# Kernel tuning notes

Measured on AMD Instinct MI355X. Metric: run time of the kernel, lower is better.

The kernel has to match this reference:

```python
import jax, jax.numpy as jnp
import numpy as np

B, T, Q, H = 128, 50, 1024, 256
MAX_STEP = 50
TEMP = 0.5
SUP_W, DIST_W, EMBED_W, LOSS_WEIGHT = 1.0, 0.01, 1.0, 1.0
BLUR, DIAMETER, REACH, SCALING, P = 0.005, 1.0, 500.0, 0.5, 2
NEG = -1e9


def _softmin(eps, C, h):
    # h: log-weights + potential/eps over the second axis of C
    return -eps * jax.nn.logsumexp(h[None, :] - C / eps, axis=1)


def _sqcost(u, v):
    sq = jnp.sum(u * u, -1)[:, None] + jnp.sum(v * v, -1)[None, :] - 2.0 * (u @ v.T)
    return 0.5 * jnp.maximum(sq, 0.0)  # geomloss p=2 cost: |x-y|^2 / 2


def sinkhorn_divergence(x, y):
    # geomloss SamplesLoss('sinkhorn', p=2, blur=0.005, diameter=1, reach=500),
    # tensorized, debiased, unbalanced, eps-scaling schedule.
    N, M = x.shape[0], y.shape[0]
    a_log = jnp.full((N,), -np.log(float(N)), dtype=x.dtype)
    b_log = jnp.full((M,), -np.log(float(M)), dtype=x.dtype)
    Cxy, Cyx = _sqcost(x, y), _sqcost(y, x)
    Cxx, Cyy = _sqcost(x, x), _sqcost(y, y)
    rho = REACH ** P
    eps_final = BLUR ** P
    eps_list = []
    e = DIAMETER ** P
    while e > eps_final:
        eps_list.append(e)
        e = e * (SCALING ** P)
    eps_list.append(eps_final)
    f_ab = jnp.zeros((N,), x.dtype)
    g_ab = jnp.zeros((M,), x.dtype)
    f_aa = jnp.zeros((N,), x.dtype)
    g_bb = jnp.zeros((M,), x.dtype)
    for eps in eps_list:  # static schedule (~9 steps)
        damp = 1.0 / (1.0 + eps / rho)
        ft = damp * _softmin(eps, Cxy, b_log + g_ab / eps)
        gt = damp * _softmin(eps, Cyx, a_log + f_ab / eps)
        faa = 0.5 * (f_aa + damp * _softmin(eps, Cxx, a_log + f_aa / eps))
        gbb = 0.5 * (g_bb + damp * _softmin(eps, Cyy, b_log + g_bb / eps))
        f_ab, g_ab, f_aa, g_bb = ft, gt, faa, gbb
    w = rho + eps_final / 2.0  # UnbalancedWeight
    a_w, b_w = jnp.exp(a_log), jnp.exp(b_log)
    return (jnp.sum(a_w * w * (jnp.exp(-f_aa / rho) - jnp.exp(-f_ab / rho)))
            + jnp.sum(b_w * w * (jnp.exp(-g_bb / rho) - jnp.exp(-g_ab / rho))))


def _forward(lc, lt, le, ltc, ltt, lte, ohs, oht, ods, odt, batch):
    p_c, p_t, p_e = lc / TEMP, lt / TEMP, le / TEMP
    q_c, q_t, q_e = ltc / TEMP, ltt / TEMP, lte / TEMP
    flat = lambda z: z.reshape(z.shape[0], -1)
    loss_kd = (sinkhorn_divergence(flat(p_c), flat(q_c))
               + sinkhorn_divergence(flat(p_t), flat(q_t))
               + sinkhorn_divergence(flat(p_e), flat(q_e)))
    S = MAX_STEP - 1
    delta = batch[:, :, :Q] + batch[:, :, Q:]  # [B,T,Q] question one-hots
    a = jnp.floor(((batch[:, :, :Q] - batch[:, :, Q:]).sum(-1) + 1.0) / 2.0)[:, 1:1 + S]  # [B,S] correctness
    dsh = delta[:, 1:1 + S]  # [B,S,Q]
    # diagonal of p[:S] @ delta[1:].T == per-step gather of next question's logit
    pc = jnp.einsum('bsq,bsq->bs', p_c[:, :S], dsh)
    pt = jnp.einsum('bsq,bsq->bs', p_t[:, :S], dsh)
    pe = jnp.einsum('bsq,bsq->bs', p_e[:, :S], dsh)
    idx = jnp.arange(S)
    last = jnp.max(jnp.where(pc > 0, idx[None, :], -1), axis=1)  # last i with pc[i] > 0
    L = jnp.where(last >= 0, last + 1, S)  # no break => keep full length
    mask = idx[None, :] < L[:, None]
    def ce(logits):
        m = jnp.where(mask, logits, NEG)
        lsm = m - jax.nn.logsumexp(m, axis=1, keepdims=True)
        return -jnp.sum(jnp.where(mask, a * lsm, 0.0))  # soft-target CE, summed over students
    loss_sup = ce(pt) + ce(pc) + ce(pe)
    embed = 0.5 * (jnp.sum((ohs - oht) ** 2) + jnp.sum((ods - odt) ** 2))
    total = LOSS_WEIGHT * (SUP_W * loss_sup + DIST_W * loss_kd + EMBED_W * embed)
    return total.reshape(1)


def setup_inputs():
    key = jax.random.key(0)
    ks = jax.random.split(key, 12)
    rn = lambda k, s: jax.random.normal(k, s, dtype=jnp.float32)
    qid = jax.random.randint(ks[10], (B, T), 0, Q)
    correct = jax.random.randint(ks[11], (B, T), 0, 2).astype(jnp.float32)
    oh = jax.nn.one_hot(qid, Q, dtype=jnp.float32)
    batch = jnp.concatenate([oh * correct[..., None], oh * (1.0 - correct)[..., None]], axis=-1)
    return {
        'logit_c': rn(ks[0], (B, T, Q)),
        'logit_t': rn(ks[1], (B, T, Q)),
        'logit_ensemble': rn(ks[2], (B, T, Q)),
        'logit_teacher_c': rn(ks[3], (B, T, Q)),
        'logit_teacher_t': rn(ks[4], (B, T, Q)),
        'logit_teacher_ensemble': rn(ks[5], (B, T, Q)),
        'out_h_student': rn(ks[6], (B, T, H)),
        'out_h_teacher': rn(ks[7], (B, T, H)),
        'out_d_student': rn(ks[8], (B, T, H)),
        'out_d_teacher': rn(ks[9], (B, T, H)),
        'batch': batch,
    }


def reference(logit_c, logit_t, logit_ensemble, logit_teacher_c, logit_teacher_t, logit_teacher_ensemble, out_h_student, out_h_teacher, out_d_student, out_d_teacher, batch):
    return _forward(logit_c, logit_t, logit_ensemble, logit_teacher_c, logit_teacher_t, logit_teacher_ensemble, out_h_student, out_h_teacher, out_d_student, out_d_teacher, batch)
```

## Files before the change

kernel.cpp:

```cpp
#include <hip/hip_runtime.h>

#define NB 128
#define T_DIM 50
#define Q_DIM 1024
#define H_DIM 256
#define S_DIM 49
#define K_DIM 51200
#define KCHUNKS 80
#define KC 640
#define BK 64
#define NSTAGE 10
#define GRAM_N (NB * NB)
#define LROWU 36
#define CPAD 132

typedef __attribute__((ext_vector_type(4))) float f32x4;
typedef __attribute__((ext_vector_type(8))) _Float16 half8v;
typedef __attribute__((ext_vector_type(4))) unsigned int uint4v;
typedef __attribute__((ext_vector_type(2))) unsigned int uint2v;
using pk2_t = decltype(__builtin_amdgcn_cvt_pkrtz(0.0f, 0.0f));

union PKU { pk2_t p; unsigned int u; };
union U4H8 { uint4v u; half8v h; };

__device__ inline unsigned short f2bf_rn(float x) {
  union { float f; unsigned int u; } v; v.f = x;
  unsigned int r = v.u + 0x7FFFu + ((v.u >> 16) & 1u);
  return (unsigned short)(r >> 16);
}
__device__ inline float bf2f(unsigned short b) {
  union { float f; unsigned int u; } v; v.u = ((unsigned int)b) << 16;
  return v.f;
}

__device__ __forceinline__ void issue_loads(
    const float* __restrict__ S, const float* __restrict__ Tm,
    size_t ro0, size_t ro1, int kpos, int kq,
    f32x4& p0, f32x4& p1, f32x4& p2, f32x4& p3) {
  const float* pS = S + kpos + kq * 4;
  const float* pT = Tm + kpos + kq * 4;
  p0 = *(const f32x4*)(pS + ro0);
  p1 = *(const f32x4*)(pS + ro1);
  p2 = *(const f32x4*)(pT + ro0);
  p3 = *(const f32x4*)(pT + ro1);
}

__device__ __forceinline__ void cvt_write(
    unsigned int* __restrict__ panA, unsigned int* __restrict__ panB,
    int r0, int kq,
    const f32x4& p0, const f32x4& p1, const f32x4& p2, const f32x4& p3) {
  PKU a, b; uint2v w;
  a.p = __builtin_amdgcn_cvt_pkrtz(p0[0], p0[1]);
  b.p = __builtin_amdgcn_cvt_pkrtz(p0[2], p0[3]);
  w.x = a.u; w.y = b.u;
  *(uint2v*)&panA[r0 * LROWU + kq * 2] = w;
  a.p = __builtin_amdgcn_cvt_pkrtz(p1[0], p1[1]);
  b.p = __builtin_amdgcn_cvt_pkrtz(p1[2], p1[3]);
  w.x = a.u; w.y = b.u;
  *(uint2v*)&panA[(r0 + 64) * LROWU + kq * 2] = w;
  a.p = __builtin_amdgcn_cvt_pkrtz(p2[0], p2[1]);
  b.p = __builtin_amdgcn_cvt_pkrtz(p2[2], p2[3]);
  w.x = a.u; w.y = b.u;
  *(uint2v*)&panB[r0 * LROWU + kq * 2] = w;
  a.p = __builtin_amdgcn_cvt_pkrtz(p3[0], p3[1]);
  b.p = __builtin_amdgcn_cvt_pkrtz(p3[2], p3[3]);
  w.x = a.u; w.y = b.u;
  *(uint2v*)&panB[(r0 + 64) * LROWU + kq * 2] = w;
}

__device__ __forceinline__ void compute_stage(
    const unsigned int* __restrict__ panA, const unsigned int* __restrict__ panB,
    int wrow, int wcol, int l15, int quad,
    f32x4 (&aXY)[2][2], f32x4 (&aXX)[2][2], f32x4 (&aYY)[2][2]) {
#pragma unroll
  for (int ks = 0; ks < 2; ks++) {
    const int kc = ks * 16 + quad * 4;
    half8v as_[2], bs_[2], at_[2], bt_[2];
#pragma unroll
    for (int t = 0; t < 2; t++) {
      U4H8 u;
      u.u = *(const uint4v*)&panA[(wrow * 32 + t * 16 + l15) * LROWU + kc]; as_[t] = u.h;
      u.u = *(const uint4v*)&panA[(wcol * 32 + t * 16 + l15) * LROWU + kc]; bs_[t] = u.h;
      u.u = *(const uint4v*)&panB[(wrow * 32 + t * 16 + l15) * LROWU + kc]; at_[t] = u.h;
      u.u = *(const uint4v*)&panB[(wcol * 32 + t * 16 + l15) * LROWU + kc]; bt_[t] = u.h;
    }
#pragma unroll
    for (int ti = 0; ti < 2; ti++)
#pragma unroll
      for (int tj = 0; tj < 2; tj++) {
        aXY[ti][tj] = __builtin_amdgcn_mfma_f32_16x16x32_f16(as_[ti], bt_[tj], aXY[ti][tj], 0, 0, 0);
        aXX[ti][tj] = __builtin_amdgcn_mfma_f32_16x16x32_f16(as_[ti], bs_[tj], aXX[ti][tj], 0, 0, 0);
        aYY[ti][tj] = __builtin_amdgcn_mfma_f32_16x16x32_f16(at_[ti], bt_[tj], aYY[ti][tj], 0, 0, 0);
      }
  }
}

__global__ __launch_bounds__(1024) void gram_fused_kernel(
    const float* __restrict__ s0, const float* __restrict__ s1, const float* __restrict__ s2,
    const float* __restrict__ t0, const float* __restrict__ t1, const float* __restrict__ t2,
    unsigned short* __restrict__ part) {
  __shared__ unsigned int pan[2][2][NB * LROWU];

  const int chunk = blockIdx.x;
  const int pair = blockIdx.y;
  const float* S  = (pair == 0) ? s0 : ((pair == 1) ? s1 : s2);
  const float* Tm = (pair == 0) ? t0 : ((pair == 1) ? t1 : t2);

  const int tid = threadIdx.x;
  const int wave = tid >> 6, lane = tid & 63;
  const int wrow = wave >> 2, wcol = wave & 3;
  const int l15 = lane & 15, quad = lane >> 4;

  f32x4 aXY[2][2], aXX[2][2], aYY[2][2];
#pragma unroll
  for (int i = 0; i < 2; i++)
#pragma unroll
    for (int j = 0; j < 2; j++) {
      aXY[i][j] = (f32x4){0.f, 0.f, 0.f, 0.f};
      aXX[i][j] = (f32x4){0.f, 0.f, 0.f, 0.f};
      aYY[i][j] = (f32x4){0.f, 0.f, 0.f, 0.f};
    }

  const int r0 = tid >> 4;
  const int kq = tid & 15;
  const size_t ro0 = (size_t)r0 * K_DIM;
  const size_t ro1 = (size_t)(r0 + 64) * K_DIM;
  const int kbase = chunk * KC;

  f32x4 A0, A1, A2, A3;
  f32x4 B0, B1, B2, B3;

  issue_loads(S, Tm, ro0, ro1, kbase, kq, A0, A1, A2, A3);
  issue_loads(S, Tm, ro0, ro1, kbase + BK, kq, B0, B1, B2, B3);
  cvt_write(&pan[0][0][0], &pan[0][1][0], r0, kq, A0, A1, A2, A3);
  __syncthreads();

  for (int s2 = 0; s2 < NSTAGE; s2 += 2) {
    if (s2 + 2 < NSTAGE)
      issue_loads(S, Tm, ro0, ro1, kbase + (s2 + 2) * BK, kq, A0, A1, A2, A3);
    compute_stage(&pan[0][0][0], &pan[0][1][0], wrow, wcol, l15, quad, aXY, aXX, aYY);
    cvt_write(&pan[1][0][0], &pan[1][1][0], r0, kq, B0, B1, B2, B3);
    __syncthreads();

    if (s2 + 3 < NSTAGE)
      issue_loads(S, Tm, ro0, ro1, kbase + (s2 + 3) * BK, kq, B0, B1, B2, B3);
    compute_stage(&pan[1][0][0], &pan[1][1][0], wrow, wcol, l15, quad, aXY, aXX, aYY);
    if (s2 + 2 < NSTAGE) {
      cvt_write(&pan[0][0][0], &pan[0][1][0], r0, kq, A0, A1, A2, A3);
      __syncthreads();
    }
  }

#pragma unroll
  for (int kind = 0; kind < 3; kind++) {
    unsigned short* out = part + ((size_t)(pair * 3 + kind) * KCHUNKS + chunk) * GRAM_N;
#pragma unroll
    for (int ti = 0; ti < 2; ti++)
#pragma unroll
      for (int tj = 0; tj < 2; tj++) {
        const f32x4 v = (kind == 0) ? aXY[ti][tj] : ((kind == 1) ? aXX[ti][tj] : aYY[ti][tj]);
        const int col = wcol * 32 + tj * 16 + l15;
#pragma unroll
        for (int r = 0; r < 4; r++) {
          const int row = wrow * 32 + ti * 16 + quad * 4 + r;
          out[(size_t)row * NB + col] = f2bf_rn(v[r]);
        }
      }
  }
}

__global__ __launch_bounds__(256) void gram_reduce_kernel(
    const unsigned short* __restrict__ part, float* __restrict__ gram) {
  const int idx = blockIdx.x * 256 + threadIdx.x;
  const int g = idx >> 14;
  const int cell = idx & (GRAM_N - 1);
  const unsigned short* p = part + (size_t)g * KCHUNKS * GRAM_N + cell;
  float s = 0.f;
#pragma unroll
  for (int c = 0; c < KCHUNKS; c++) s += bf2f(p[(size_t)c * GRAM_N]);
  gram[idx] = s;
}

__global__ __launch_bounds__(256, 1) void sinkhorn_part_kernel(
    const float* __restrict__ gram, float* __restrict__ kdpart) {
  const int pair = blockIdx.x, kind = blockIdx.y;
  const float* Gxy = gram + (size_t)(3 * pair + 0) * GRAM_N;
  const float* Gxx = gram + (size_t)(3 * pair + 1) * GRAM_N;
  const float* Gyy = gram + (size_t)(3 * pair + 2) * GRAM_N;

  __shared__ float CL[NB * CPAD];
  __shared__ f32x4 h4a[NB / 4];
  __shared__ f32x4 h4b[NB / 4];
  __shared__ float nx[NB], ny[NB];
  __shared__ float red[256];

  const int tid = threadIdx.x;
  if (tid < NB) {
    nx[tid] = Gxx[tid * (NB + 1)];
    ny[tid] = Gyy[tid * (NB + 1)];
    ((float*)h4a)[tid] = 0.f;
    ((float*)h4b)[tid] = 0.f;
  }
  __syncthreads();

  const float* G  = (kind == 0) ? Gxy : ((kind == 1) ? Gxx : Gyy);
  const float* rn = (kind == 2) ? ny : nx;
  const float* cn = (kind == 1) ? nx : ny;
  for (int idx = tid; idx < GRAM_N; idx += 256) {
    const int i = idx >> 7, j = idx & 127;
    CL[i * CPAD + j] = 2.0f * fmaxf(rn[i] + cn[j] - 2.0f * G[idx], 0.0f);
  }
  __syncthreads();

  const float rho = 250000.0f;
  const float AL = -4.852030263919617f;
  const float LOG2E = 1.4426950408889634f;
  const float LN2 = 0.6931471805599453f;
  const int grp = tid >> 7;
  const int i = tid & 127;
  const bool active = (kind == 0) || (grp == 0);
  const bool colread = (kind == 0) && (grp == 1);

  f32x4 crow[32];
  if (active) {
    if (colread) {
#pragma unroll
      for (int jj = 0; jj < 32; jj++) {
        f32x4 v;
        v[0] = CL[(4 * jj + 0) * CPAD + i];
        v[1] = CL[(4 * jj + 1) * CPAD + i];
        v[2] = CL[(4 * jj + 2) * CPAD + i];
        v[3] = CL[(4 * jj + 3) * CPAD + i];
        crow[jj] = v;
      }
    } else {
#pragma unroll
      for (int jj = 0; jj < 32; jj++)
        crow[jj] = *(const f32x4*)&CL[i * CPAD + 4 * jj];
    }
  }

  float eps = 1.0f;
  for (int it = 0; it < 9; it++) {
    if (it == 8) eps = 2.5e-5f;
    const float inv_eps = 1.0f / eps;
    const float damp = 1.0f / (1.0f + eps / rho);
    const float ebl = eps * AL;

    float newp = 0.f;
    if (active) {
      const f32x4* h = (kind == 0 && grp == 0) ? h4b : h4a;
      f32x4 m4 = (f32x4){-3.0e38f, -3.0e38f, -3.0e38f, -3.0e38f};
#pragma unroll
      for (int jj = 0; jj < 32; jj++) {
        const f32x4 u = h[jj] - crow[jj];
        m4[0] = fmaxf(m4[0], u[0]); m4[1] = fmaxf(m4[1], u[1]);
        m4[2] = fmaxf(m4[2], u[2]); m4[3] = fmaxf(m4[3], u[3]);
      }
      const float m = fmaxf(fmaxf(m4[0], m4[1]), fmaxf(m4[2], m4[3]));
      const float k = inv_eps * LOG2E;
      f32x4 s4 = (f32x4){0.f, 0.f, 0.f, 0.f};
#pragma unroll
      for (int jj = 0; jj < 32; jj++) {
        const f32x4 u = h[jj] - crow[jj];
        s4[0] += __builtin_exp2f((u[0] - m) * k);
        s4[1] += __builtin_exp2f((u[1] - m) * k);
        s4[2] += __builtin_exp2f((u[2] - m) * k);
        s4[3] += __builtin_exp2f((u[3] - m) * k);
      }
      const float Ssum = (s4[0] + s4[1]) + (s4[2] + s4[3]);
      const float sm = -(m + ebl + eps * (LN2 * __log2f(Ssum)));
      if (kind == 0) newp = damp * sm;
      else           newp = 0.5f * (((const float*)h4a)[i] + damp * sm);
    }
    __syncthreads();
    if (active) {
      if (grp == 0) ((float*)h4a)[i] = newp;
      else          ((float*)h4b)[i] = newp;
    }
    __syncthreads();
    eps *= 0.25f;
  }

  float v = 0.f;
  if (kind == 0) {
    v = (grp == 0) ? -__expf(-((const float*)h4a)[i] / rho)
                   : -__expf(-((const float*)h4b)[i] / rho);
  } else if (grp == 0) {
    v = __expf(-((const float*)h4a)[i] / rho);
  }
  red[tid] = v;
  __syncthreads();
  for (int st = 128; st > 0; st >>= 1) {
    if (tid < st) red[tid] += red[tid + st];
    __syncthreads();
  }
  if (tid == 0) kdpart[pair * 3 + kind] = red[0];
}

__global__ __launch_bounds__(256) void ps_kernel(
    const float* __restrict__ lc, const float* __restrict__ lt, const float* __restrict__ le,
    const float* __restrict__ batch,
    float* __restrict__ pc, float* __restrict__ pt, float* __restrict__ pe,
    float* __restrict__ aarr) {
  const int w = blockIdx.x * 4 + (threadIdx.x >> 6);
  if (w >= NB * S_DIM) return;
  const int lane = threadIdx.x & 63;
  const int b = w / S_DIM, s = w - b * S_DIM;
  const float* brow = batch + ((size_t)b * T_DIM + (s + 1)) * (2 * Q_DIM);

  int qv = 0; float dsv = 0.f; bool found = false;
#pragma unroll
  for (int c = 0; c < 4; c++) {
    const int base = c * 256 + lane * 4;
    const f32x4 d0 = *(const f32x4*)(brow + base);
    const f32x4 d1 = *(const f32x4*)(brow + Q_DIM + base);
#pragma unroll
    for (int j = 0; j < 4; j++)
      if (d0[j] + d1[j] > 0.5f) { qv = base + j; dsv = d0[j] - d1[j]; found = true; }
  }
  const unsigned long long m = __ballot(found);
  const int src = (m != 0ull) ? (__ffsll((unsigned long long)m) - 1) : 0;
  qv = __shfl(qv, src, 64);
  dsv = __shfl(dsv, src, 64);
  if (lane == 0) {
    const size_t off = ((size_t)b * T_DIM + s) * Q_DIM + qv;
    pc[w] = 2.0f * lc[off];
    pt[w] = 2.0f * lt[off];
    pe[w] = 2.0f * le[off];
    aarr[w] = (m != 0ull && dsv > 0.0f) ? 1.0f : 0.0f;
  }
}

__global__ __launch_bounds__(256) void embed_kernel(
    const f32x4* __restrict__ hs, const f32x4* __restrict__ ht,
    const f32x4* __restrict__ ds, const f32x4* __restrict__ dt,
    float* __restrict__ acc) {
  const int N4 = NB * T_DIM * H_DIM / 4;
  float sum = 0.f;
  for (int idx = blockIdx.x * 256 + threadIdx.x; idx < N4; idx += gridDim.x * 256) {
    f32x4 a = hs[idx] - ht[idx];
    f32x4 b = ds[idx] - dt[idx];
    sum += a[0]*a[0] + a[1]*a[1] + a[2]*a[2] + a[3]*a[3]
         + b[0]*b[0] + b[1]*b[1] + b[2]*b[2] + b[3]*b[3];
  }
  for (int off = 32; off > 0; off >>= 1) sum += __shfl_down(sum, off, 64);
  __shared__ float wsum[4];
  const int lane = threadIdx.x & 63, wv = threadIdx.x >> 6;
  if (lane == 0) wsum[wv] = sum;
  __syncthreads();
  if (threadIdx.x == 0) atomicAdd(acc, wsum[0] + wsum[1] + wsum[2] + wsum[3]);
}

__global__ __launch_bounds__(128) void ce_final_kernel(
    const float* __restrict__ pc, const float* __restrict__ pt, const float* __restrict__ pe,
    const float* __restrict__ aarr, const float* __restrict__ kdpart,
    const float* __restrict__ emb, float* __restrict__ out) {
  __shared__ float sx[4][NB][S_DIM];
  const int tid = threadIdx.x;
  for (int idx = tid; idx < NB * S_DIM; idx += 128) {
    const int b = idx / S_DIM, s = idx - b * S_DIM;
    sx[0][b][s] = pt[idx];
    sx[1][b][s] = pc[idx];
    sx[2][b][s] = pe[idx];
    sx[3][b][s] = aarr[idx];
  }
  __syncthreads();

  const int b = tid;
  int last = -1;
  for (int s = 0; s < S_DIM; s++)
    if (sx[1][b][s] > 0.0f) last = s;
  const int L = (last >= 0) ? (last + 1) : S_DIM;

  float loss = 0.f;
#pragma unroll
  for (int k = 0; k < 3; k++) {
    float m = -3.0e38f;
    for (int s = 0; s < L; s++) m = fmaxf(m, sx[k][b][s]);
    float sum = 0.f;
    for (int s = 0; s < L; s++) sum += __expf(sx[k][b][s] - m);
    const float lse = m + __logf(sum);
    float l = 0.f;
    for (int s = 0; s < L; s++) l += sx[3][b][s] * (sx[k][b][s] - lse);
    loss -= l;
  }

  __shared__ float red[128];
  red[b] = loss;
  __syncthreads();
  for (int st = 64; st > 0; st >>= 1) {
    if (b < st) red[b] += red[b + st];
    __syncthreads();
  }
  if (b == 0) {
    float kd = 0.f;
    for (int k = 0; k < 9; k++) kd += kdpart[k];
    out[0] = red[0] + 0.01f * (250000.0000125f / 128.0f) * kd + 0.5f * emb[0];
  }
}

extern "C" void kernel_launch(void* const* d_in, const int* in_sizes, int n_in,
                              void* d_out, int out_size, void* d_ws, size_t ws_size,
                              hipStream_t stream) {
  const float* lc    = (const float*)d_in[0];
  const float* lt    = (const float*)d_in[1];
  const float* le    = (const float*)d_in[2];
  const float* ltc   = (const float*)d_in[3];
  const float* ltt   = (const float*)d_in[4];
  const float* lte   = (const float*)d_in[5];
  const float* ohs   = (const float*)d_in[6];
  const float* oht   = (const float*)d_in[7];
  const float* ods   = (const float*)d_in[8];
  const float* odt   = (const float*)d_in[9];
  const float* batch = (const float*)d_in[10];

  unsigned short* part = (unsigned short*)d_ws;
  float* gram = (float*)(part + (size_t)9 * KCHUNKS * GRAM_N);
  float* pcb  = gram + 9 * GRAM_N;
  float* ptb  = pcb + NB * S_DIM;
  float* peb  = ptb + NB * S_DIM;
  float* ab   = peb + NB * S_DIM;
  float* kdp  = ab + NB * S_DIM;
  float* emb  = kdp + 9;

  hipMemsetAsync(emb, 0, sizeof(float), stream);

  embed_kernel<<<1600, 256, 0, stream>>>(
      (const f32x4*)ohs, (const f32x4*)oht, (const f32x4*)ods, (const f32x4*)odt, emb);

  ps_kernel<<<(NB * S_DIM + 3) / 4, 256, 0, stream>>>(lc, lt, le, batch, pcb, ptb, peb, ab);

  gram_fused_kernel<<<dim3(KCHUNKS, 3), 1024, 0, stream>>>(lc, lt, le, ltc, ltt, lte, part);

  gram_reduce_kernel<<<(9 * GRAM_N) / 256, 256, 0, stream>>>(part, gram);

  sinkhorn_part_kernel<<<dim3(3, 3), 256, 0, stream>>>(gram, kdp);

  ce_final_kernel<<<1, 128, 0, stream>>>(pcb, ptb, peb, ab, kdp, emb, (float*)d_out);
}
```

Measured before the change: 342.9 us.

## Split gram kernel output rows across two 512-thread blocks per chunk

New measurement: 353.9 us. +3.2%, slower.

```diff
diff --git a/kernel.cpp b/kernel.cpp
--- a/kernel.cpp
+++ b/kernel.cpp
@@ -33,44 +33,38 @@
   return v.f;
 }
 
-__device__ __forceinline__ void issue_loads(
+__device__ __forceinline__ void issue_loads2(
     const float* __restrict__ S, const float* __restrict__ Tm,
-    size_t ro0, size_t ro1, int kpos, int kq,
-    f32x4& p0, f32x4& p1, f32x4& p2, f32x4& p3) {
-  const float* pS = S + kpos + kq * 4;
-  const float* pT = Tm + kpos + kq * 4;
-  p0 = *(const f32x4*)(pS + ro0);
-  p1 = *(const f32x4*)(pS + ro1);
-  p2 = *(const f32x4*)(pT + ro0);
-  p3 = *(const f32x4*)(pT + ro1);
-}
-
-__device__ __forceinline__ void cvt_write(
+    size_t ro, int kpos,
+    f32x4 (&pS)[4], f32x4 (&pT)[4]) {
+#pragma unroll
+  for (int j = 0; j < 4; j++) {
+    pS[j] = *(const f32x4*)(S + ro + kpos + j * 16);
+    pT[j] = *(const f32x4*)(Tm + ro + kpos + j * 16);
+  }
+}
+
+__device__ __forceinline__ void cvt_write2(
     unsigned int* __restrict__ panA, unsigned int* __restrict__ panB,
-    int r0, int kq,
-    const f32x4& p0, const f32x4& p1, const f32x4& p2, const f32x4& p3) {
-  PKU a, b; uint2v w;
-  a.p = __builtin_amdgcn_cvt_pkrtz(p0[0], p0[1]);
-  b.p = __builtin_amdgcn_cvt_pkrtz(p0[2], p0[3]);
-  w.x = a.u; w.y = b.u;
-  *(uint2v*)&panA[r0 * LROWU + kq * 2] = w;
-  a.p = __builtin_amdgcn_cvt_pkrtz(p1[0], p1[1]);
-  b.p = __builtin_amdgcn_cvt_pkrtz(p1[2], p1[3]);
-  w.x = a.u; w.y = b.u;
-  *(uint2v*)&panA[(r0 + 64) * LROWU + kq * 2] = w;
-  a.p = __builtin_amdgcn_cvt_pkrtz(p2[0], p2[1]);
-  b.p = __builtin_amdgcn_cvt_pkrtz(p2[2], p2[3]);
-  w.x = a.u; w.y = b.u;
-  *(uint2v*)&panB[r0 * LROWU + kq * 2] = w;
-  a.p = __builtin_amdgcn_cvt_pkrtz(p3[0], p3[1]);
-  b.p = __builtin_amdgcn_cvt_pkrtz(p3[2], p3[3]);
-  w.x = a.u; w.y = b.u;
-  *(uint2v*)&panB[(r0 + 64) * LROWU + kq * 2] = w;
-}
-
-__device__ __forceinline__ void compute_stage(
+    int r0, int q,
+    const f32x4 (&pS)[4], const f32x4 (&pT)[4]) {
+#pragma unroll
+  for (int j = 0; j < 4; j++) {
+    PKU a, b; uint2v w;
+    a.p = __builtin_amdgcn_cvt_pkrtz(pS[j][0], pS[j][1]);
+    b.p = __builtin_amdgcn_cvt_pkrtz(pS[j][2], pS[j][3]);
+    w.x = a.u; w.y = b.u;
+    *(uint2v*)&panA[r0 * LROWU + q * 2 + j * 8] = w;
+    a.p = __builtin_amdgcn_cvt_pkrtz(pT[j][0], pT[j][1]);
+    b.p = __builtin_amdgcn_cvt_pkrtz(pT[j][2], pT[j][3]);
+    w.x = a.u; w.y = b.u;
+    *(uint2v*)&panB[r0 * LROWU + q * 2 + j * 8] = w;
+  }
+}
+
+__device__ __forceinline__ void compute_stage2(
     const unsigned int* __restrict__ panA, const unsigned int* __restrict__ panB,
-    int wrow, int wcol, int l15, int quad,
+    int rowbase, int wcol, int l15, int quad,
     f32x4 (&aXY)[2][2], f32x4 (&aXX)[2][2], f32x4 (&aYY)[2][2]) {
 #pragma unroll
   for (int ks = 0; ks < 2; ks++) {
@@ -79,9 +73,9 @@
 #pragma unroll
     for (int t = 0; t < 2; t++) {
       U4H8 u;
-      u.u = *(const uint4v*)&panA[(wrow * 32 + t * 16 + l15) * LROWU + kc]; as_[t] = u.h;
+      u.u = *(const uint4v*)&panA[(rowbase + t * 16 + l15) * LROWU + kc];   as_[t] = u.h;
       u.u = *(const uint4v*)&panA[(wcol * 32 + t * 16 + l15) * LROWU + kc]; bs_[t] = u.h;
-      u.u = *(const uint4v*)&panB[(wrow * 32 + t * 16 + l15) * LROWU + kc]; at_[t] = u.h;
+      u.u = *(const uint4v*)&panB[(rowbase + t * 16 + l15) * LROWU + kc];   at_[t] = u.h;
       u.u = *(const uint4v*)&panB[(wcol * 32 + t * 16 + l15) * LROWU + kc]; bt_[t] = u.h;
     }
 #pragma unroll
@@ -95,21 +89,24 @@
   }
 }
 
-__global__ __launch_bounds__(1024) void gram_fused_kernel(
+__global__ __launch_bounds__(512) void gram_fused_kernel(
     const float* __restrict__ s0, const float* __restrict__ s1, const float* __restrict__ s2,
     const float* __restrict__ t0, const float* __restrict__ t1, const float* __restrict__ t2,
     unsigned short* __restrict__ part) {
   __shared__ unsigned int pan[2][2][NB * LROWU];
 
   const int chunk = blockIdx.x;
-  const int pair = blockIdx.y;
+  const int hblk = blockIdx.y;
+  const int pair = blockIdx.z;
   const float* S  = (pair == 0) ? s0 : ((pair == 1) ? s1 : s2);
   const float* Tm = (pair == 0) ? t0 : ((pair == 1) ? t1 : t2);
 
   const int tid = threadIdx.x;
   const int wave = tid >> 6, lane = tid & 63;
-  const int wrow = wave >> 2, wcol = wave & 3;
+  const int wrow = wave >> 2;
+  const int wcol = wave & 3;
   const int l15 = lane & 15, quad = lane >> 4;
+  const int rowbase = hblk * 64 + wrow * 32;
 
   f32x4 aXY[2][2], aXX[2][2], aYY[2][2];
 #pragma unroll
@@ -121,32 +118,23 @@
       aYY[i][j] = (f32x4){0.f, 0.f, 0.f, 0.f};
     }
 
-  const int r0 = tid >> 4;
-  const int kq = tid & 15;
-  const size_t ro0 = (size_t)r0 * K_DIM;
-  const size_t ro1 = (size_t)(r0 + 64) * K_DIM;
+  const int r0 = tid >> 2;
+  const int q  = tid & 3;
+  const size_t ro = (size_t)r0 * K_DIM + q * 4;
   const int kbase = chunk * KC;
 
-  f32x4 A0, A1, A2, A3;
-  f32x4 B0, B1, B2, B3;
-
-  issue_loads(S, Tm, ro0, ro1, kbase, kq, A0, A1, A2, A3);
-  issue_loads(S, Tm, ro0, ro1, kbase + BK, kq, B0, B1, B2, B3);
-  cvt_write(&pan[0][0][0], &pan[0][1][0], r0, kq, A0, A1, A2, A3);
-  __syncthreads();
-
-  for (int s2 = 0; s2 < NSTAGE; s2 += 2) {
-    if (s2 + 2 < NSTAGE)
-      issue_loads(S, Tm, ro0, ro1, kbase + (s2 + 2) * BK, kq, A0, A1, A2, A3);
-    compute_stage(&pan[0][0][0], &pan[0][1][0], wrow, wcol, l15, quad, aXY, aXX, aYY);
-    cvt_write(&pan[1][0][0], &pan[1][1][0], r0, kq, B0, B1, B2, B3);
-    __syncthreads();
-
-    if (s2 + 3 < NSTAGE)
-      issue_loads(S, Tm, ro0, ro1, kbase + (s2 + 3) * BK, kq, B0, B1, B2, B3);
-    compute_stage(&pan[1][0][0], &pan[1][1][0], wrow, wcol, l15, quad, aXY, aXX, aYY);
-    if (s2 + 2 < NSTAGE) {
-      cvt_write(&pan[0][0][0], &pan[0][1][0], r0, kq, A0, A1, A2, A3);
+  f32x4 pS[4], pT[4];
+
+  issue_loads2(S, Tm, ro, kbase, pS, pT);
+  cvt_write2(&pan[0][0][0], &pan[0][1][0], r0, q, pS, pT);
+  __syncthreads();
+
+  for (int st = 0; st < NSTAGE; st++) {
+    const int buf = st & 1;
+    if (st + 1 < NSTAGE) issue_loads2(S, Tm, ro, kbase + (st + 1) * BK, pS, pT);
+    compute_stage2(&pan[buf][0][0], &pan[buf][1][0], rowbase, wcol, l15, quad, aXY, aXX, aYY);
+    if (st + 1 < NSTAGE) {
+      cvt_write2(&pan[buf ^ 1][0][0], &pan[buf ^ 1][1][0], r0, q, pS, pT);
       __syncthreads();
     }
   }
@@ -162,7 +150,7 @@
         const int col = wcol * 32 + tj * 16 + l15;
 #pragma unroll
         for (int r = 0; r < 4; r++) {
-          const int row = wrow * 32 + ti * 16 + quad * 4 + r;
+          const int row = rowbase + ti * 16 + quad * 4 + r;
           out[(size_t)row * NB + col] = f2bf_rn(v[r]);
         }
       }
@@ -431,7 +419,7 @@
 
   ps_kernel<<<(NB * S_DIM + 3) / 4, 256, 0, stream>>>(lc, lt, le, batch, pcb, ptb, peb, ab);
 
-  gram_fused_kernel<<<dim3(KCHUNKS, 3), 1024, 0, stream>>>(lc, lt, le, ltc, ltt, lte, part);
+  gram_fused_kernel<<<dim3(KCHUNKS, 2, 3), 512, 0, stream>>>(lc, lt, le, ltc, ltt, lte, part);
 
   gram_reduce_kernel<<<(9 * GRAM_N) / 256, 256, 0, stream>>>(part, gram);
 
```

## Pre-convert logits to fp16 tiled panels before Gram MFMA kernel

Applied to the files above, without the earlier changes.

New measurement: 420.4 us. +22.6%, slower.

```diff
diff --git a/kernel.cpp b/kernel.cpp
--- a/kernel.cpp
+++ b/kernel.cpp
@@ -13,6 +13,8 @@
 #define GRAM_N (NB * NB)
 #define LROWU 36
 #define CPAD 132
+#define NTILE 800
+#define TSTRU 4160
 
 typedef __attribute__((ext_vector_type(4))) float f32x4;
 typedef __attribute__((ext_vector_type(8))) _Float16 half8v;
@@ -31,6 +33,141 @@
 __device__ inline float bf2f(unsigned short b) {
   union { float f; unsigned int u; } v; v.u = ((unsigned int)b) << 16;
   return v.f;
+}
+
+__global__ __launch_bounds__(256) void convert_kernel(
+    const float* __restrict__ s0, const float* __restrict__ s1, const float* __restrict__ s2,
+    const float* __restrict__ t0, const float* __restrict__ t1, const float* __restrict__ t2,
+    unsigned int* __restrict__ tiles) {
+  const int m = blockIdx.x >> 7;
+  const int r = blockIdx.x & 127;
+  const float* src = (m == 0) ? s0 : (m == 1) ? s1 : (m == 2) ? s2
+                   : (m == 3) ? t0 : (m == 4) ? t1 : t2;
+  const float* row = src + (size_t)r * K_DIM;
+  unsigned int* base = tiles + (size_t)m * NTILE * TSTRU;
+  const int t = threadIdx.x;
+#pragma unroll
+  for (int i = 0; i < 4; i++) {
+    const int w = i * 256 + t;
+    if (w < NTILE) {
+      const float* pk = row + w * 64;
+      unsigned int* dst = base + (size_t)w * TSTRU + r * 32;
+#pragma unroll
+      for (int j = 0; j < 8; j++) {
+        const f32x4 a = *(const f32x4*)(pk + j * 8);
+        const f32x4 b = *(const f32x4*)(pk + j * 8 + 4);
+        PKU u0, u1, u2, u3;
+        u0.p = __builtin_amdgcn_cvt_pkrtz(a[0], a[1]);
+        u1.p = __builtin_amdgcn_cvt_pkrtz(a[2], a[3]);
+        u2.p = __builtin_amdgcn_cvt_pkrtz(b[0], b[1]);
+        u3.p = __builtin_amdgcn_cvt_pkrtz(b[2], b[3]);
+        uint4v wv; wv.x = u0.u; wv.y = u1.u; wv.z = u2.u; wv.w = u3.u;
+        *(uint4v*)(dst + j * 4) = wv;
+      }
+    }
+  }
+}
+
+__device__ __forceinline__ void compute_stage(
+    const unsigned int* __restrict__ panA, const unsigned int* __restrict__ panB,
+    int wrow, int wcol, int l15, int quad,
+    f32x4 (&aXY)[2][2], f32x4 (&aXX)[2][2], f32x4 (&aYY)[2][2]) {
+#pragma unroll
+  for (int ks = 0; ks < 2; ks++) {
+    const int kc = ks * 16 + quad * 4;
+    half8v as_[2], bs_[2], at_[2], bt_[2];
+#pragma unroll
+    for (int t = 0; t < 2; t++) {
+      U4H8 u;
+      u.u = *(const uint4v*)&panA[(wrow * 32 + t * 16 + l15) * LROWU + kc]; as_[t] = u.h;
+      u.u = *(const uint4v*)&panA[(wcol * 32 + t * 16 + l15) * LROWU + kc]; bs_[t] = u.h;
+      u.u = *(const uint4v*)&panB[(wrow * 32 + t * 16 + l15) * LROWU + kc]; at_[t] = u.h;
+      u.u = *(const uint4v*)&panB[(wcol * 32 + t * 16 + l15) * LROWU + kc]; bt_[t] = u.h;
+    }
+#pragma unroll
+    for (int ti = 0; ti < 2; ti++)
+#pragma unroll
+      for (int tj = 0; tj < 2; tj++) {
+        aXY[ti][tj] = __builtin_amdgcn_mfma_f32_16x16x32_f16(as_[ti], bt_[tj], aXY[ti][tj], 0, 0, 0);
+        aXX[ti][tj] = __builtin_amdgcn_mfma_f32_16x16x32_f16(as_[ti], bs_[tj], aXX[ti][tj], 0, 0, 0);
+        aYY[ti][tj] = __builtin_amdgcn_mfma_f32_16x16x32_f16(at_[ti], bt_[tj], aYY[ti][tj], 0, 0, 0);
+      }
+  }
+}
+
+__global__ __launch_bounds__(1024) void gram_tiles_kernel(
+    const unsigned int* __restrict__ tiles, unsigned short* __restrict__ part) {
+  __shared__ unsigned int pan[2][2][NB * LROWU];
+
+  const int chunk = blockIdx.x;
+  const int pair = blockIdx.y;
+  const unsigned int* tS = tiles + (size_t)pair * NTILE * TSTRU;
+  const unsigned int* tT = tiles + (size_t)(pair + 3) * NTILE * TSTRU;
+
+  const int tid = threadIdx.x;
+  const int wave = tid >> 6, lane = tid & 63;
+  const int wrow = wave >> 2, wcol = wave & 3;
+  const int l15 = lane & 15, quad = lane >> 4;
+
+  f32x4 aXY[2][2], aXX[2][2], aYY[2][2];
+#pragma unroll
+  for (int i = 0; i < 2; i++)
+#pragma unroll
+    for (int j = 0; j < 2; j++) {
+      aXY[i][j] = (f32x4){0.f, 0.f, 0.f, 0.f};
+      aXX[i][j] = (f32x4){0.f, 0.f, 0.f, 0.f};
+      aYY[i][j] = (f32x4){0.f, 0.f, 0.f, 0.f};
+    }
+
+  const int r0 = tid >> 3;
+  const int h  = tid & 7;
+  const size_t soff = (size_t)tid * 4;
+
+  uint4v pS, pT;
+#define ISSUE(ST)                                                     \
+  {                                                                   \
+    const size_t tb = (size_t)(chunk * NSTAGE + (ST)) * TSTRU;        \
+    pS = *(const uint4v*)(tS + tb + soff);                            \
+    pT = *(const uint4v*)(tT + tb + soff);                            \
+  }
+#define WRITE(BUF)                                                    \
+  {                                                                   \
+    *(uint4v*)&pan[BUF][0][r0 * LROWU + h * 4] = pS;                  \
+    *(uint4v*)&pan[BUF][1][r0 * LROWU + h * 4] = pT;                  \
+  }
+
+  ISSUE(0)
+  WRITE(0)
+  __syncthreads();
+
+  for (int st = 0; st < NSTAGE; st++) {
+    const int buf = st & 1;
+    if (st + 1 < NSTAGE) ISSUE(st + 1)
+    compute_stage(&pan[buf][0][0], &pan[buf][1][0], wrow, wcol, l15, quad, aXY, aXX, aYY);
+    if (st + 1 < NSTAGE) {
+      WRITE(buf ^ 1)
+      __syncthreads();
+    }
+  }
+#undef ISSUE
+#undef WRITE
+
+#pragma unroll
+  for (int kind = 0; kind < 3; kind++) {
+    unsigned short* out = part + ((size_t)(pair * 3 + kind) * KCHUNKS + chunk) * GRAM_N;
+#pragma unroll
+    for (int ti = 0; ti < 2; ti++)
+#pragma unroll
+      for (int tj = 0; tj < 2; tj++) {
+        const f32x4 v = (kind == 0) ? aXY[ti][tj] : ((kind == 1) ? aXX[ti][tj] : aYY[ti][tj]);
+        const int col = wcol * 32 + tj * 16 + l15;
+#pragma unroll
+        for (int r = 0; r < 4; r++) {
+          const int row = wrow * 32 + ti * 16 + quad * 4 + r;
+          out[(size_t)row * NB + col] = f2bf_rn(v[r]);
+        }
+      }
+  }
 }
 
 __device__ __forceinline__ void issue_loads(
@@ -68,34 +205,7 @@
   *(uint2v*)&panB[(r0 + 64) * LROWU + kq * 2] = w;
 }
 
-__device__ __forceinline__ void compute_stage(
-    const unsigned int* __restrict__ panA, const unsigned int* __restrict__ panB,
-    int wrow, int wcol, int l15, int quad,
-    f32x4 (&aXY)[2][2], f32x4 (&aXX)[2][2], f32x4 (&aYY)[2][2]) {
-#pragma unroll
-  for (int ks = 0; ks < 2; ks++) {
-    const int kc = ks * 16 + quad * 4;
-    half8v as_[2], bs_[2], at_[2], bt_[2];
-#pragma unroll
-    for (int t = 0; t < 2; t++) {
-      U4H8 u;
-      u.u = *(const uint4v*)&panA[(wrow * 32 + t * 16 + l15) * LROWU + kc]; as_[t] = u.h;
-      u.u = *(const uint4v*)&panA[(wcol * 32 + t * 16 + l15) * LROWU + kc]; bs_[t] = u.h;
-      u.u = *(const uint4v*)&panB[(wrow * 32 + t * 16 + l15) * LROWU + kc]; at_[t] = u.h;
-      u.u = *(const uint4v*)&panB[(wcol * 32 + t * 16 + l15) * LROWU + kc]; bt_[t] = u.h;
-    }
-#pragma unroll
-    for (int ti = 0; ti < 2; ti++)
-#pragma unroll
-      for (int tj = 0; tj < 2; tj++) {
-        aXY[ti][tj] = __builtin_amdgcn_mfma_f32_16x16x32_f16(as_[ti], bt_[tj], aXY[ti][tj], 0, 0, 0);
-        aXX[ti][tj] = __builtin_amdgcn_mfma_f32_16x16x32_f16(as_[ti], bs_[tj], aXX[ti][tj], 0, 0, 0);
-        aYY[ti][tj] = __builtin_amdgcn_mfma_f32_16x16x32_f16(at_[ti], bt_[tj], aYY[ti][tj], 0, 0, 0);
-      }
-  }
-}
-
-__global__ __launch_bounds__(1024) void gram_fused_kernel(
+__global__ __launch_bounds__(1024) void gram_fused_legacy(
     const float* __restrict__ s0, const float* __restrict__ s1, const float* __restrict__ s2,
     const float* __restrict__ t0, const float* __restrict__ t1, const float* __restrict__ t2,
     unsigned short* __restrict__ part) {
@@ -127,8 +237,7 @@
   const size_t ro1 = (size_t)(r0 + 64) * K_DIM;
   const int kbase = chunk * KC;
 
-  f32x4 A0, A1, A2, A3;
-  f32x4 B0, B1, B2, B3;
+  f32x4 A0, A1, A2, A3, B0, B1, B2, B3;
 
   issue_loads(S, Tm, ro0, ro1, kbase, kq, A0, A1, A2, A3);
   issue_loads(S, Tm, ro0, ro1, kbase + BK, kq, B0, B1, B2, B3);
@@ -415,8 +524,16 @@
   const float* odt   = (const float*)d_in[9];
   const float* batch = (const float*)d_in[10];
 
-  unsigned short* part = (unsigned short*)d_ws;
-  float* gram = (float*)(part + (size_t)9 * KCHUNKS * GRAM_N);
+  const size_t tilesBytes = (size_t)6 * NTILE * TSTRU * 4;
+  const size_t partBytes  = (size_t)9 * KCHUNKS * GRAM_N * 2;
+  const size_t tailBytes  = ((size_t)9 * GRAM_N + 4 * NB * S_DIM + 16) * 4;
+  const bool useTiles = (ws_size >= tilesBytes + partBytes + tailBytes);
+
+  unsigned int* tiles = (unsigned int*)d_ws;
+  unsigned short* part = useTiles
+      ? (unsigned short*)((char*)d_ws + tilesBytes)
+      : (unsigned short*)d_ws;
+  float* gram = (float*)((char*)part + partBytes);
   float* pcb  = gram + 9 * GRAM_N;
   float* ptb  = pcb + NB * S_DIM;
   float* peb  = ptb + NB * S_DIM;
@@ -431,7 +548,12 @@
 
   ps_kernel<<<(NB * S_DIM + 3) / 4, 256, 0, stream>>>(lc, lt, le, batch, pcb, ptb, peb, ab);
 
-  gram_fused_kernel<<<dim3(KCHUNKS, 3), 1024, 0, stream>>>(lc, lt, le, ltc, ltt, lte, part);
+  if (useTiles) {
+    convert_kernel<<<6 * NB, 256, 0, stream>>>(lc, lt, le, ltc, ltt, lte, tiles);
+    gram_tiles_kernel<<<dim3(KCHUNKS, 3), 1024, 0, stream>>>(tiles, part);
+  } else {
+    gram_fused_legacy<<<dim3(KCHUNKS, 3), 1024, 0, stream>>>(lc, lt, le, ltc, ltt, lte, part);
+  }
 
   gram_reduce_kernel<<<(9 * GRAM_N) / 256, 256, 0, stream>>>(part, gram);
 
```
